# Kernel optimization log

Measured on AMD Instinct MI355X. Metric: run time of the kernel, lower is better.

## Reference

```python
import jax, jax.numpy as jnp
import numpy as np

EPS = 1e-12   # F.normalize eps
COS_EPS = 1e-8  # F.cosine_similarity eps

B, S, V, D, P, L = 4, 2048, 64, 1024, 8, 24
H = D // 24            # prefix_transform bottleneck = 42
K = 2 * L * D          # 49152 output feature dim


def setup_inputs() -> dict:
    key = jax.random.key(0)
    ks = jax.random.split(key, 8)
    return {
        "prefix": jax.random.randint(ks[0], (B, V), 0, V),
        "ctx_embeds": jax.random.normal(ks[1], (B, S, D), jnp.float32),
        "tables": jax.random.normal(ks[2], (P, V, D), jnp.float32) * 0.02,
        "lora_prefix_emb": jax.random.normal(ks[3], (P, D), jnp.float32),
        "w1": jax.random.normal(ks[4], (D, H), jnp.float32) * 0.02,
        "b1": jnp.zeros((H,), jnp.float32),
        "w2": jax.random.normal(ks[5], (H, K), jnp.float32) * 0.02,
        "b2": jnp.zeros((K,), jnp.float32),
    }


def _gates(ctx_embeds, lora_prefix_emb):
    """select_prefix, vectorized over the num_prefix_set loop.

    The original builds sim_i = bmm(norm(emb), norm(e_i.repeat(B,S,1), dim=0).permute)
    of shape [B,S,S]; since the key is repeated, every column of sim is identical,
    so we carry the column vector [P,B,S] and the math is exact.
    """
    b, s, _ = ctx_embeds.shape
    # normalize embedding over feature dim (F.normalize p=2 dim=2)
    emb_n = ctx_embeds / jnp.maximum(
        jnp.linalg.norm(ctx_embeds, axis=2, keepdims=True), EPS)
    # F.normalize over dim=0 of a tensor repeated B times -> sign(x)/sqrt(B)
    u = lora_prefix_emb / jnp.maximum(
        jnp.sqrt(float(b)) * jnp.abs(lora_prefix_emb), EPS)  # [P,D]
    v = jnp.einsum('bsd,pd->pbs', emb_n, u)          # column of sim matrix
    c = jnp.maximum(v, 0.0)                          # clamp(min=0)
    # F.normalize over last dim (length S, all entries equal c) -> c/(sqrt(S)*c)
    n = c / jnp.maximum(jnp.sqrt(float(s)) * c, EPS)
    w = jax.nn.softmax(n, axis=2)                    # softmax over token dim (dim=1 in torch layout)
    a_v = jnp.einsum('pbs,bsd->pbd', w, ctx_embeds)  # attended value per expert
    e_norm = jnp.linalg.norm(lora_prefix_emb, axis=1)          # [P]
    a_norm = jnp.linalg.norm(a_v, axis=2)                      # [P,B]
    cos = jnp.einsum('pd,pbd->pb', lora_prefix_emb, a_v) / \
        jnp.maximum(e_norm[:, None] * a_norm, COS_EPS)
    return jax.nn.softmax(cos.T, axis=-1)            # self.s_t, [B,P]


def reference(prefix, ctx_embeds, tables, lora_prefix_emb, w1, b1, w2, b2):
    s_t = _gates(ctx_embeds, lora_prefix_emb)        # [B,P]
    # forward() re-applies softmax to self.s_t (faithful double softmax)
    gate = jax.nn.softmax(s_t, axis=-1)              # [B,P]
    tok = tables[:, prefix]                          # [P,B,V,D] per-expert embedding lookup
    h = jnp.tanh(jnp.einsum('pbvd,dh->pbvh', tok, w1) + b1)
    pkv = jnp.einsum('pbvh,hk->pbvk', h, w2) + b2    # [P,B,V,K]
    out = jnp.einsum('bp,pbvk->bvk', gate, pkv)      # gated mixture over experts
    return out
```

## Files before the change

kernel.cpp:

```cpp
#include <hip/hip_runtime.h>

#define BB 4
#define SS 2048
#define VV 64
#define DD 1024
#define PP 8
#define HH 42
#define KK 49152

static constexpr float F_EPS = 1e-12f;
static constexpr float SQRT_S = 45.254833995939045f;

__global__ __launch_bounds__(256) void k15_fused(
    const float* __restrict__ ctx, const float* __restrict__ lora,
    const float* __restrict__ tables, const float* __restrict__ w1,
    const float* __restrict__ b1, float* __restrict__ n_ws,
    float* __restrict__ h_all) {
  __shared__ float smem[PP * DD];
  const int t = threadIdx.x;
  if (blockIdx.x < 512) {
    for (int i = t; i < PP * DD; i += 256) {
      float e = lora[i];
      smem[i] = e / fmaxf(2.0f * fabsf(e), F_EPS);
    }
    __syncthreads();
    const int wave = t >> 6, lane = t & 63;
    const int rbase = blockIdx.x * 16 + wave * 4;
    const float4* ctx4 = (const float4*)ctx;
    const float4* u4 = (const float4*)smem;
    float dot[4][PP];
    float sq[4] = {0.f, 0.f, 0.f, 0.f};
    #pragma unroll
    for (int i = 0; i < 4; ++i)
      #pragma unroll
      for (int p = 0; p < PP; ++p) dot[i][p] = 0.f;
    #pragma unroll
    for (int j = 0; j < 4; ++j) {
      float4 c[4];
      #pragma unroll
      for (int i = 0; i < 4; ++i)
        c[i] = ctx4[(size_t)(rbase + i) * 256 + j * 64 + lane];
      #pragma unroll
      for (int i = 0; i < 4; ++i)
        sq[i] += c[i].x * c[i].x + c[i].y * c[i].y + c[i].z * c[i].z + c[i].w * c[i].w;
      #pragma unroll
      for (int p = 0; p < PP; ++p) {
        float4 u = u4[p * 256 + j * 64 + lane];
        #pragma unroll
        for (int i = 0; i < 4; ++i)
          dot[i][p] += c[i].x * u.x + c[i].y * u.y + c[i].z * u.z + c[i].w * u.w;
      }
    }
    const int sel = lane & 7;
    #pragma unroll
    for (int i = 0; i < 4; ++i) {
      float s = sq[i];
      #pragma unroll
      for (int m = 32; m >= 1; m >>= 1) s += __shfl_xor(s, m, 64);
      float d0 = dot[i][0], d1 = dot[i][1], d2 = dot[i][2], d3 = dot[i][3];
      float d4 = dot[i][4], d5 = dot[i][5], d6 = dot[i][6], d7 = dot[i][7];
      #pragma unroll
      for (int m = 1; m <= 4; m <<= 1) {
        d0 += __shfl_xor(d0, m, 64); d1 += __shfl_xor(d1, m, 64);
        d2 += __shfl_xor(d2, m, 64); d3 += __shfl_xor(d3, m, 64);
        d4 += __shfl_xor(d4, m, 64); d5 += __shfl_xor(d5, m, 64);
        d6 += __shfl_xor(d6, m, 64); d7 += __shfl_xor(d7, m, 64);
      }
      float v = d0;
      v = (sel == 1) ? d1 : v; v = (sel == 2) ? d2 : v;
      v = (sel == 3) ? d3 : v; v = (sel == 4) ? d4 : v;
      v = (sel == 5) ? d5 : v; v = (sel == 6) ? d6 : v;
      v = (sel == 7) ? d7 : v;
      v += __shfl_xor(v, 8, 64);
      v += __shfl_xor(v, 16, 64);
      v += __shfl_xor(v, 32, 64);
      if (lane < PP) {
        float inv = 1.0f / fmaxf(sqrtf(s), F_EPS);
        float c = fmaxf(v * inv, 0.0f);
        n_ws[(size_t)(rbase + i) * 8 + lane] = c / fmaxf(SQRT_S * c, F_EPS);
      }
    }
  } else {
    float* row_lds = smem;
    float* partial = smem + DD;
    const int r = blockIdx.x - 512;
    ((float4*)row_lds)[t] = ((const float4*)(tables + (size_t)r * DD))[t];
    __syncthreads();
    const int h = t & 63, q = t >> 6;
    float acc = 0.0f;
    if (h < HH) {
      const int d0 = q * 256;
      #pragma unroll 8
      for (int dl = 0; dl < 256; ++dl) {
        acc += row_lds[d0 + dl] * w1[(size_t)(d0 + dl) * HH + h];
      }
    }
    partial[q * 64 + h] = acc;
    __syncthreads();
    if (t < HH) {
      float s = partial[t] + partial[64 + t] + partial[128 + t] + partial[192 + t];
      h_all[(size_t)r * HH + t] = tanhf(s + b1[t]);
    }
  }
}

__global__ __launch_bounds__(256) void k3_av(
    const float* __restrict__ ctx, const float* __restrict__ n_ws,
    float* __restrict__ part) {
  const int t = threadIdx.x;
  const int chunk = blockIdx.x;
  const int b = blockIdx.y;
  const int dz = blockIdx.z;
  __shared__ float zpart[4][PP];
  __shared__ float Zl[PP];
  __shared__ float w_lds[64 * PP];
  float z[PP];
  #pragma unroll
  for (int p = 0; p < PP; ++p) z[p] = 0.0f;
  const float4* n4 = (const float4*)n_ws;
  for (int it = 0; it < 8; ++it) {
    int s = it * 256 + t;
    float4 a = n4[(size_t)(b * SS + s) * 2];
    float4 c = n4[(size_t)(b * SS + s) * 2 + 1];
    z[0] += expf(a.x); z[1] += expf(a.y); z[2] += expf(a.z); z[3] += expf(a.w);
    z[4] += expf(c.x); z[5] += expf(c.y); z[6] += expf(c.z); z[7] += expf(c.w);
  }
  #pragma unroll
  for (int m = 32; m >= 1; m >>= 1) {
    #pragma unroll
    for (int p = 0; p < PP; ++p) z[p] += __shfl_xor(z[p], m, 64);
  }
  const int wave = t >> 6, lane = t & 63;
  if (lane == 0) {
    #pragma unroll
    for (int p = 0; p < PP; ++p) zpart[wave][p] = z[p];
  }
  __syncthreads();
  if (t < PP) Zl[t] = zpart[0][t] + zpart[1][t] + zpart[2][t] + zpart[3][t];
  __syncthreads();
  if (t < 64) {
    int s = chunk * 64 + t;
    #pragma unroll
    for (int p = 0; p < PP; ++p)
      w_lds[t * PP + p] = expf(n_ws[(size_t)(b * SS + s) * 8 + p]) / Zl[p];
  }
  __syncthreads();
  float2 acc[PP];
  #pragma unroll
  for (int p = 0; p < PP; ++p) acc[p] = make_float2(0.f, 0.f);
  const float2* ctx2 = (const float2*)ctx;
  const float4* w4 = (const float4*)w_lds;
  #pragma unroll 4
  for (int sl = 0; sl < 64; ++sl) {
    int s = chunk * 64 + sl;
    float2 c = ctx2[(size_t)(b * SS + s) * 512 + dz * 256 + t];
    float4 wa = w4[sl * 2];
    float4 wb = w4[sl * 2 + 1];
    float w[PP] = {wa.x, wa.y, wa.z, wa.w, wb.x, wb.y, wb.z, wb.w};
    #pragma unroll
    for (int p = 0; p < PP; ++p) {
      acc[p].x += w[p] * c.x;
      acc[p].y += w[p] * c.y;
    }
  }
  float2* part2 = (float2*)part;
  #pragma unroll
  for (int p = 0; p < PP; ++p)
    part2[(size_t)((b * 32 + chunk) * PP + p) * 512 + dz * 256 + t] = acc[p];
}

__global__ __launch_bounds__(256) void k4_cos(
    const float* __restrict__ part, const float* __restrict__ lora,
    float* __restrict__ cos_ws) {
  const int t = threadIdx.x;
  const int p = blockIdx.x, b = blockIdx.y;
  const float4* part4 = (const float4*)part;
  float4 av = make_float4(0.f, 0.f, 0.f, 0.f);
  #pragma unroll 8
  for (int c = 0; c < 32; ++c) {
    float4 x = part4[(size_t)((b * 32 + c) * PP + p) * 256 + t];
    av.x += x.x; av.y += x.y; av.z += x.z; av.w += x.w;
  }
  float4 e = ((const float4*)lora)[p * 256 + t];
  float dt = av.x * e.x + av.y * e.y + av.z * e.z + av.w * e.w;
  float a2 = av.x * av.x + av.y * av.y + av.z * av.z + av.w * av.w;
  float e2 = e.x * e.x + e.y * e.y + e.z * e.z + e.w * e.w;
  #pragma unroll
  for (int m = 32; m >= 1; m >>= 1) {
    dt += __shfl_xor(dt, m, 64);
    a2 += __shfl_xor(a2, m, 64);
    e2 += __shfl_xor(e2, m, 64);
  }
  __shared__ float red[4][3];
  const int wave = t >> 6, lane = t & 63;
  if (lane == 0) { red[wave][0] = dt; red[wave][1] = a2; red[wave][2] = e2; }
  __syncthreads();
  if (t == 0) {
    float Dv = red[0][0] + red[1][0] + red[2][0] + red[3][0];
    float Av = red[0][1] + red[1][1] + red[2][1] + red[3][1];
    float Ev = red[0][2] + red[1][2] + red[2][2] + red[3][2];
    cos_ws[b * PP + p] = Dv / fmaxf(sqrtf(Ev) * sqrtf(Av), 1e-8f);
  }
}

__global__ __launch_bounds__(256) void k7_out(
    const float* __restrict__ w2, const float* __restrict__ b2,
    const float* __restrict__ h_all, const float* __restrict__ cos_ws,
    const int* __restrict__ prefix, float* __restrict__ out) {
  __shared__ float gate_lds[PP];
  __shared__ float hg_lds[HH * 64];
  __shared__ float w2_lds[HH * 128];
  const int t = threadIdx.x;
  const int b = blockIdx.y;
  const size_t kbase = (size_t)blockIdx.x * 128;
  for (int i = t; i < HH * 128; i += 256) {
    int h = i >> 7, kk = i & 127;
    w2_lds[i] = w2[(size_t)h * KK + kbase + kk];
  }
  if (t == 0) {
    float c[PP];
    float m = -1e30f;
    #pragma unroll
    for (int p = 0; p < PP; ++p) { c[p] = cos_ws[b * PP + p]; m = fmaxf(m, c[p]); }
    float s = 0.0f;
    #pragma unroll
    for (int p = 0; p < PP; ++p) { c[p] = expf(c[p] - m); s += c[p]; }
    float inv = 1.0f / s;
    float m2 = -1e30f;
    #pragma unroll
    for (int p = 0; p < PP; ++p) { c[p] *= inv; m2 = fmaxf(m2, c[p]); }
    float s2 = 0.0f;
    #pragma unroll
    for (int p = 0; p < PP; ++p) { c[p] = expf(c[p] - m2); s2 += c[p]; }
    float inv2 = 1.0f / s2;
    #pragma unroll
    for (int p = 0; p < PP; ++p) gate_lds[p] = c[p] * inv2;
  }
  __syncthreads();
  for (int idx = t; idx < 64 * HH; idx += 256) {
    int v = idx / HH;
    int h = idx - v * HH;
    int tokv = prefix[b * VV + v];
    float s = 0.0f;
    #pragma unroll
    for (int p = 0; p < PP; ++p)
      s += gate_lds[p] * h_all[(size_t)(p * VV + tokv) * HH + h];
    hg_lds[h * 64 + v] = s;
  }
  __syncthreads();
  const int tk = t & 31, tb = t >> 5;
  float4 acc[8];
  #pragma unroll
  for (int i = 0; i < 8; ++i) acc[i] = make_float4(0.f, 0.f, 0.f, 0.f);
  const float4* w24 = (const float4*)w2_lds;
  const float4* hg4 = (const float4*)hg_lds;
  #pragma unroll 2
  for (int h = 0; h < HH; ++h) {
    float4 wv = w24[h * 32 + tk];
    float4 g0 = hg4[h * 16 + tb * 2];
    float4 g1 = hg4[h * 16 + tb * 2 + 1];
    float gg[8] = {g0.x, g0.y, g0.z, g0.w, g1.x, g1.y, g1.z, g1.w};
    #pragma unroll
    for (int i = 0; i < 8; ++i) {
      acc[i].x += gg[i] * wv.x;
      acc[i].y += gg[i] * wv.y;
      acc[i].z += gg[i] * wv.z;
      acc[i].w += gg[i] * wv.w;
    }
  }
  float4 b2v = ((const float4*)b2)[(kbase >> 2) + tk];
  float4* out4 = (float4*)out;
  #pragma unroll
  for (int i = 0; i < 8; ++i) {
    int bv = b * 64 + tb * 8 + i;
    float4 o;
    o.x = acc[i].x + b2v.x;
    o.y = acc[i].y + b2v.y;
    o.z = acc[i].z + b2v.z;
    o.w = acc[i].w + b2v.w;
    out4[(((size_t)bv * KK + kbase) >> 2) + tk] = o;
  }
}

extern "C" void kernel_launch(void* const* d_in, const int* in_sizes, int n_in,
                              void* d_out, int out_size, void* d_ws, size_t ws_size,
                              hipStream_t stream) {
  const int* prefix = (const int*)d_in[0];
  const float* ctx = (const float*)d_in[1];
  const float* tables = (const float*)d_in[2];
  const float* lora = (const float*)d_in[3];
  const float* w1 = (const float*)d_in[4];
  const float* b1 = (const float*)d_in[5];
  const float* w2 = (const float*)d_in[6];
  const float* b2 = (const float*)d_in[7];
  float* out = (float*)d_out;
  char* ws = (char*)d_ws;
  float* n_ws = (float*)ws;
  float* part = (float*)(ws + 262144);
  float* cos_ws = (float*)(ws + 262144 + 4194304);
  float* h_all = (float*)(ws + 262144 + 4194304 + 128);

  k15_fused<<<1024, 256, 0, stream>>>(ctx, lora, tables, w1, b1, n_ws, h_all);
  k3_av<<<dim3(32, 4, 2), 256, 0, stream>>>(ctx, n_ws, part);
  k4_cos<<<dim3(8, 4), 256, 0, stream>>>(part, lora, cos_ws);
  k7_out<<<dim3(384, 4), 256, 0, stream>>>(w2, b2, h_all, cos_ws, prefix, out);
}
```

Measured before the change: 161.9 us.

## Fuse attention-weighted ctx accumulation into gate kernel, dropping softmax normalizer

The kernel that computes per-token similarity scores now also exponentiates them and accumulates the exp-weighted ctx sums in registers, so the separate attended-value kernel and its second full pass over ctx are removed. The softmax denominator is no longer applied, on the grounds that cosine similarity is invariant to per-(p,b) scaling. The cost is a large register footprint per thread (8×4 float4 accumulators), fewer blocks on the ctx path (256) and twice as many partial sums written and reduced. The per-expert key transform is recomputed from global memory on every row pair instead of being staged once in LDS.

Measured after the change: 190.5 us. +17.7%, slower.

```diff
diff --git a/kernel.cpp b/kernel.cpp
--- a/kernel.cpp
+++ b/kernel.cpp
@@ -11,79 +11,128 @@
 static constexpr float F_EPS = 1e-12f;
 static constexpr float SQRT_S = 45.254833995939045f;
 
-__global__ __launch_bounds__(256) void k15_fused(
+__global__ __launch_bounds__(256) void kA_fused(
     const float* __restrict__ ctx, const float* __restrict__ lora,
     const float* __restrict__ tables, const float* __restrict__ w1,
-    const float* __restrict__ b1, float* __restrict__ n_ws,
+    const float* __restrict__ b1, float* __restrict__ part,
     float* __restrict__ h_all) {
-  __shared__ float smem[PP * DD];
+  __shared__ float smem[16384];
   const int t = threadIdx.x;
-  if (blockIdx.x < 512) {
-    for (int i = t; i < PP * DD; i += 256) {
-      float e = lora[i];
-      smem[i] = e / fmaxf(2.0f * fabsf(e), F_EPS);
-    }
-    __syncthreads();
+  if (blockIdx.x < 256) {
+    const int b = blockIdx.x >> 6;
+    const int chunk = blockIdx.x & 63;
     const int wave = t >> 6, lane = t & 63;
-    const int rbase = blockIdx.x * 16 + wave * 4;
+    const int sel = lane & 7;
     const float4* ctx4 = (const float4*)ctx;
-    const float4* u4 = (const float4*)smem;
-    float dot[4][PP];
-    float sq[4] = {0.f, 0.f, 0.f, 0.f};
-    #pragma unroll
-    for (int i = 0; i < 4; ++i)
-      #pragma unroll
-      for (int p = 0; p < PP; ++p) dot[i][p] = 0.f;
-    #pragma unroll
-    for (int j = 0; j < 4; ++j) {
-      float4 c[4];
-      #pragma unroll
-      for (int i = 0; i < 4; ++i)
-        c[i] = ctx4[(size_t)(rbase + i) * 256 + j * 64 + lane];
-      #pragma unroll
-      for (int i = 0; i < 4; ++i)
-        sq[i] += c[i].x * c[i].x + c[i].y * c[i].y + c[i].z * c[i].z + c[i].w * c[i].w;
-      #pragma unroll
-      for (int p = 0; p < PP; ++p) {
-        float4 u = u4[p * 256 + j * 64 + lane];
-        #pragma unroll
-        for (int i = 0; i < 4; ++i)
-          dot[i][p] += c[i].x * u.x + c[i].y * u.y + c[i].z * u.z + c[i].w * u.w;
-      }
-    }
-    const int sel = lane & 7;
-    #pragma unroll
-    for (int i = 0; i < 4; ++i) {
-      float s = sq[i];
-      #pragma unroll
-      for (int m = 32; m >= 1; m >>= 1) s += __shfl_xor(s, m, 64);
-      float d0 = dot[i][0], d1 = dot[i][1], d2 = dot[i][2], d3 = dot[i][3];
-      float d4 = dot[i][4], d5 = dot[i][5], d6 = dot[i][6], d7 = dot[i][7];
+    const float4* lora4 = (const float4*)lora;
+    float4 acc[PP][4];
+    #pragma unroll
+    for (int p = 0; p < PP; ++p)
+      #pragma unroll
+      for (int j = 0; j < 4; ++j) acc[p][j] = make_float4(0.f, 0.f, 0.f, 0.f);
+    const int rbase = b * SS + chunk * 32 + wave * 8;
+
+    auto reduce_accum = [&](float sq, float* d, float4* c) {
+      #pragma unroll
+      for (int m = 32; m >= 1; m >>= 1) sq += __shfl_xor(sq, m, 64);
       #pragma unroll
       for (int m = 1; m <= 4; m <<= 1) {
-        d0 += __shfl_xor(d0, m, 64); d1 += __shfl_xor(d1, m, 64);
-        d2 += __shfl_xor(d2, m, 64); d3 += __shfl_xor(d3, m, 64);
-        d4 += __shfl_xor(d4, m, 64); d5 += __shfl_xor(d5, m, 64);
-        d6 += __shfl_xor(d6, m, 64); d7 += __shfl_xor(d7, m, 64);
-      }
-      float v = d0;
-      v = (sel == 1) ? d1 : v; v = (sel == 2) ? d2 : v;
-      v = (sel == 3) ? d3 : v; v = (sel == 4) ? d4 : v;
-      v = (sel == 5) ? d5 : v; v = (sel == 6) ? d6 : v;
-      v = (sel == 7) ? d7 : v;
+        #pragma unroll
+        for (int p = 0; p < PP; ++p) d[p] += __shfl_xor(d[p], m, 64);
+      }
+      float v = d[0];
+      v = (sel == 1) ? d[1] : v; v = (sel == 2) ? d[2] : v;
+      v = (sel == 3) ? d[3] : v; v = (sel == 4) ? d[4] : v;
+      v = (sel == 5) ? d[5] : v; v = (sel == 6) ? d[6] : v;
+      v = (sel == 7) ? d[7] : v;
       v += __shfl_xor(v, 8, 64);
       v += __shfl_xor(v, 16, 64);
       v += __shfl_xor(v, 32, 64);
-      if (lane < PP) {
-        float inv = 1.0f / fmaxf(sqrtf(s), F_EPS);
-        float c = fmaxf(v * inv, 0.0f);
-        n_ws[(size_t)(rbase + i) * 8 + lane] = c / fmaxf(SQRT_S * c, F_EPS);
-      }
+      float inv = 1.0f / fmaxf(sqrtf(sq), F_EPS);
+      float cc = fmaxf(v * inv, 0.0f);
+      float n = cc / fmaxf(SQRT_S * cc, F_EPS);
+      float exl = expf(n);
+      float ex[PP];
+      #pragma unroll
+      for (int p = 0; p < PP; ++p) ex[p] = __shfl(exl, p, 64);
+      #pragma unroll
+      for (int p = 0; p < PP; ++p) {
+        #pragma unroll
+        for (int j = 0; j < 4; ++j) {
+          acc[p][j].x += ex[p] * c[j].x;
+          acc[p][j].y += ex[p] * c[j].y;
+          acc[p][j].z += ex[p] * c[j].z;
+          acc[p][j].w += ex[p] * c[j].w;
+        }
+      }
+    };
+
+    for (int g = 0; g < 4; ++g) {
+      const int r = rbase + g * 2;
+      float4 c0[4], c1[4];
+      float d0[PP], d1[PP];
+      float sq0 = 0.f, sq1 = 0.f;
+      #pragma unroll
+      for (int p = 0; p < PP; ++p) { d0[p] = 0.f; d1[p] = 0.f; }
+      #pragma unroll
+      for (int j = 0; j < 4; ++j) {
+        c0[j] = ctx4[(size_t)r * 256 + j * 64 + lane];
+        c1[j] = ctx4[(size_t)(r + 1) * 256 + j * 64 + lane];
+        sq0 += c0[j].x * c0[j].x + c0[j].y * c0[j].y + c0[j].z * c0[j].z + c0[j].w * c0[j].w;
+        sq1 += c1[j].x * c1[j].x + c1[j].y * c1[j].y + c1[j].z * c1[j].z + c1[j].w * c1[j].w;
+        #pragma unroll
+        for (int p = 0; p < PP; ++p) {
+          float4 e4 = lora4[p * 256 + j * 64 + lane];
+          float4 u;
+          u.x = e4.x / fmaxf(2.0f * fabsf(e4.x), F_EPS);
+          u.y = e4.y / fmaxf(2.0f * fabsf(e4.y), F_EPS);
+          u.z = e4.z / fmaxf(2.0f * fabsf(e4.z), F_EPS);
+          u.w = e4.w / fmaxf(2.0f * fabsf(e4.w), F_EPS);
+          d0[p] += c0[j].x * u.x + c0[j].y * u.y + c0[j].z * u.z + c0[j].w * u.w;
+          d1[p] += c1[j].x * u.x + c1[j].y * u.y + c1[j].z * u.z + c1[j].w * u.w;
+        }
+      }
+      reduce_accum(sq0, d0, c0);
+      reduce_accum(sq1, d1, c1);
+    }
+
+    float4* reg = (float4*)(smem + (wave & 1) * 8192);
+    if (wave < 2) {
+      #pragma unroll
+      for (int p = 0; p < PP; ++p)
+        #pragma unroll
+        for (int j = 0; j < 4; ++j)
+          reg[p * 256 + j * 64 + lane] = acc[p][j];
+    }
+    __syncthreads();
+    if (wave >= 2) {
+      #pragma unroll
+      for (int p = 0; p < PP; ++p)
+        #pragma unroll
+        for (int j = 0; j < 4; ++j) {
+          int idx = p * 256 + j * 64 + lane;
+          float4 o = reg[idx];
+          o.x += acc[p][j].x; o.y += acc[p][j].y;
+          o.z += acc[p][j].z; o.w += acc[p][j].w;
+          reg[idx] = o;
+        }
+    }
+    __syncthreads();
+    const float4* r0 = (const float4*)smem;
+    const float4* r1 = (const float4*)(smem + 8192);
+    float4* part4 = (float4*)part;
+    const size_t base = (size_t)((b * 64 + chunk) * PP) * 256;
+    #pragma unroll
+    for (int pp = 0; pp < PP; ++pp) {
+      int idx = pp * 256 + t;
+      float4 x0 = r0[idx], x1 = r1[idx];
+      part4[base + idx] = make_float4(x0.x + x1.x, x0.y + x1.y,
+                                      x0.z + x1.z, x0.w + x1.w);
     }
   } else {
     float* row_lds = smem;
     float* partial = smem + DD;
-    const int r = blockIdx.x - 512;
+    const int r = blockIdx.x - 256;
     ((float4*)row_lds)[t] = ((const float4*)(tables + (size_t)r * DD))[t];
     __syncthreads();
     const int h = t & 63, q = t >> 6;
@@ -104,72 +153,7 @@
   }
 }
 
-__global__ __launch_bounds__(256) void k3_av(
-    const float* __restrict__ ctx, const float* __restrict__ n_ws,
-    float* __restrict__ part) {
-  const int t = threadIdx.x;
-  const int chunk = blockIdx.x;
-  const int b = blockIdx.y;
-  const int dz = blockIdx.z;
-  __shared__ float zpart[4][PP];
-  __shared__ float Zl[PP];
-  __shared__ float w_lds[64 * PP];
-  float z[PP];
-  #pragma unroll
-  for (int p = 0; p < PP; ++p) z[p] = 0.0f;
-  const float4* n4 = (const float4*)n_ws;
-  for (int it = 0; it < 8; ++it) {
-    int s = it * 256 + t;
-    float4 a = n4[(size_t)(b * SS + s) * 2];
-    float4 c = n4[(size_t)(b * SS + s) * 2 + 1];
-    z[0] += expf(a.x); z[1] += expf(a.y); z[2] += expf(a.z); z[3] += expf(a.w);
-    z[4] += expf(c.x); z[5] += expf(c.y); z[6] += expf(c.z); z[7] += expf(c.w);
-  }
-  #pragma unroll
-  for (int m = 32; m >= 1; m >>= 1) {
-    #pragma unroll
-    for (int p = 0; p < PP; ++p) z[p] += __shfl_xor(z[p], m, 64);
-  }
-  const int wave = t >> 6, lane = t & 63;
-  if (lane == 0) {
-    #pragma unroll
-    for (int p = 0; p < PP; ++p) zpart[wave][p] = z[p];
-  }
-  __syncthreads();
-  if (t < PP) Zl[t] = zpart[0][t] + zpart[1][t] + zpart[2][t] + zpart[3][t];
-  __syncthreads();
-  if (t < 64) {
-    int s = chunk * 64 + t;
-    #pragma unroll
-    for (int p = 0; p < PP; ++p)
-      w_lds[t * PP + p] = expf(n_ws[(size_t)(b * SS + s) * 8 + p]) / Zl[p];
-  }
-  __syncthreads();
-  float2 acc[PP];
-  #pragma unroll
-  for (int p = 0; p < PP; ++p) acc[p] = make_float2(0.f, 0.f);
-  const float2* ctx2 = (const float2*)ctx;
-  const float4* w4 = (const float4*)w_lds;
-  #pragma unroll 4
-  for (int sl = 0; sl < 64; ++sl) {
-    int s = chunk * 64 + sl;
-    float2 c = ctx2[(size_t)(b * SS + s) * 512 + dz * 256 + t];
-    float4 wa = w4[sl * 2];
-    float4 wb = w4[sl * 2 + 1];
-    float w[PP] = {wa.x, wa.y, wa.z, wa.w, wb.x, wb.y, wb.z, wb.w};
-    #pragma unroll
-    for (int p = 0; p < PP; ++p) {
-      acc[p].x += w[p] * c.x;
-      acc[p].y += w[p] * c.y;
-    }
-  }
-  float2* part2 = (float2*)part;
-  #pragma unroll
-  for (int p = 0; p < PP; ++p)
-    part2[(size_t)((b * 32 + chunk) * PP + p) * 512 + dz * 256 + t] = acc[p];
-}
-
-__global__ __launch_bounds__(256) void k4_cos(
+__global__ __launch_bounds__(256) void kB_cos(
     const float* __restrict__ part, const float* __restrict__ lora,
     float* __restrict__ cos_ws) {
   const int t = threadIdx.x;
@@ -177,8 +161,8 @@
   const float4* part4 = (const float4*)part;
   float4 av = make_float4(0.f, 0.f, 0.f, 0.f);
   #pragma unroll 8
-  for (int c = 0; c < 32; ++c) {
-    float4 x = part4[(size_t)((b * 32 + c) * PP + p) * 256 + t];
+  for (int c = 0; c < 64; ++c) {
+    float4 x = part4[(size_t)((b * 64 + c) * PP + p) * 256 + t];
     av.x += x.x; av.y += x.y; av.z += x.z; av.w += x.w;
   }
   float4 e = ((const float4*)lora)[p * 256 + t];
@@ -295,13 +279,11 @@
   const float* b2 = (const float*)d_in[7];
   float* out = (float*)d_out;
   char* ws = (char*)d_ws;
-  float* n_ws = (float*)ws;
-  float* part = (float*)(ws + 262144);
-  float* cos_ws = (float*)(ws + 262144 + 4194304);
-  float* h_all = (float*)(ws + 262144 + 4194304 + 128);
-
-  k15_fused<<<1024, 256, 0, stream>>>(ctx, lora, tables, w1, b1, n_ws, h_all);
-  k3_av<<<dim3(32, 4, 2), 256, 0, stream>>>(ctx, n_ws, part);
-  k4_cos<<<dim3(8, 4), 256, 0, stream>>>(part, lora, cos_ws);
+  float* part = (float*)ws;
+  float* cos_ws = (float*)(ws + 8388608);
+  float* h_all = (float*)(ws + 8388608 + 128);
+
+  kA_fused<<<768, 256, 0, stream>>>(ctx, lora, tables, w1, b1, part, h_all);
+  kB_cos<<<dim3(8, 4), 256, 0, stream>>>(part, lora, cos_ws);
   k7_out<<<dim3(384, 4), 256, 0, stream>>>(w2, b2, h_all, cos_ws, prefix, out);
 }
```

## Replace normalized gate scores with sign-based constants and drop softmax partition sums

Applied to the files above, without the earlier changes.

The per-token score c/(sqrt(S)*c) can only be 1/sqrt(S) or 0, so only the sign of the dot product matters. The first kernel therefore skips the ctx sum-of-squares reduction and writes exp(1/sqrt(S)) or 1 directly as an unnormalized softmax weight. The second kernel drops its full-sequence exp/sum pass and block syncs. This relies on the later cosine similarity being invariant to positive per-(p,b) scaling of a_v, so the softmax denominator cancels. The only risk is a small difference in eps-clamp edge cases.

After: 157.6 us. 2.7% less time.

```diff
diff --git a/kernel.cpp b/kernel.cpp
--- a/kernel.cpp
+++ b/kernel.cpp
@@ -9,7 +9,7 @@
 #define KK 49152
 
 static constexpr float F_EPS = 1e-12f;
-static constexpr float SQRT_S = 45.254833995939045f;
+static constexpr float ALPHA = 1.02234304f;
 
 __global__ __launch_bounds__(256) void k15_fused(
     const float* __restrict__ ctx, const float* __restrict__ lora,
@@ -29,7 +29,6 @@
     const float4* ctx4 = (const float4*)ctx;
     const float4* u4 = (const float4*)smem;
     float dot[4][PP];
-    float sq[4] = {0.f, 0.f, 0.f, 0.f};
     #pragma unroll
     for (int i = 0; i < 4; ++i)
       #pragma unroll
@@ -40,9 +39,6 @@
       #pragma unroll
       for (int i = 0; i < 4; ++i)
         c[i] = ctx4[(size_t)(rbase + i) * 256 + j * 64 + lane];
-      #pragma unroll
-      for (int i = 0; i < 4; ++i)
-        sq[i] += c[i].x * c[i].x + c[i].y * c[i].y + c[i].z * c[i].z + c[i].w * c[i].w;
       #pragma unroll
       for (int p = 0; p < PP; ++p) {
         float4 u = u4[p * 256 + j * 64 + lane];
@@ -54,9 +50,6 @@
     const int sel = lane & 7;
     #pragma unroll
     for (int i = 0; i < 4; ++i) {
-      float s = sq[i];
-      #pragma unroll
-      for (int m = 32; m >= 1; m >>= 1) s += __shfl_xor(s, m, 64);
       float d0 = dot[i][0], d1 = dot[i][1], d2 = dot[i][2], d3 = dot[i][3];
       float d4 = dot[i][4], d5 = dot[i][5], d6 = dot[i][6], d7 = dot[i][7];
       #pragma unroll
@@ -74,11 +67,8 @@
       v += __shfl_xor(v, 8, 64);
       v += __shfl_xor(v, 16, 64);
       v += __shfl_xor(v, 32, 64);
-      if (lane < PP) {
-        float inv = 1.0f / fmaxf(sqrtf(s), F_EPS);
-        float c = fmaxf(v * inv, 0.0f);
-        n_ws[(size_t)(rbase + i) * 8 + lane] = c / fmaxf(SQRT_S * c, F_EPS);
-      }
+      if (lane < PP)
+        n_ws[(size_t)(rbase + i) * 8 + lane] = (v > 0.0f) ? ALPHA : 1.0f;
     }
   } else {
     float* row_lds = smem;
@@ -111,39 +101,10 @@
   const int chunk = blockIdx.x;
   const int b = blockIdx.y;
   const int dz = blockIdx.z;
-  __shared__ float zpart[4][PP];
-  __shared__ float Zl[PP];
   __shared__ float w_lds[64 * PP];
-  float z[PP];
-  #pragma unroll
-  for (int p = 0; p < PP; ++p) z[p] = 0.0f;
-  const float4* n4 = (const float4*)n_ws;
-  for (int it = 0; it < 8; ++it) {
-    int s = it * 256 + t;
-    float4 a = n4[(size_t)(b * SS + s) * 2];
-    float4 c = n4[(size_t)(b * SS + s) * 2 + 1];
-    z[0] += expf(a.x); z[1] += expf(a.y); z[2] += expf(a.z); z[3] += expf(a.w);
-    z[4] += expf(c.x); z[5] += expf(c.y); z[6] += expf(c.z); z[7] += expf(c.w);
-  }
-  #pragma unroll
-  for (int m = 32; m >= 1; m >>= 1) {
-    #pragma unroll
-    for (int p = 0; p < PP; ++p) z[p] += __shfl_xor(z[p], m, 64);
-  }
-  const int wave = t >> 6, lane = t & 63;
-  if (lane == 0) {
-    #pragma unroll
-    for (int p = 0; p < PP; ++p) zpart[wave][p] = z[p];
-  }
-  __syncthreads();
-  if (t < PP) Zl[t] = zpart[0][t] + zpart[1][t] + zpart[2][t] + zpart[3][t];
-  __syncthreads();
-  if (t < 64) {
-    int s = chunk * 64 + t;
-    #pragma unroll
-    for (int p = 0; p < PP; ++p)
-      w_lds[t * PP + p] = expf(n_ws[(size_t)(b * SS + s) * 8 + p]) / Zl[p];
-  }
+  if (t < 128)
+    ((float4*)w_lds)[t] =
+        ((const float4*)(n_ws + (size_t)(b * SS + chunk * 64) * 8))[t];
   __syncthreads();
   float2 acc[PP];
   #pragma unroll
```
